# Kernel tuning notes

Hardware: AMD Instinct MI355X
Metric: run time of the kernel (lower is better)

## Reference

```python
import jax, jax.numpy as jnp
import numpy as np

B, U = 64, 512            # batch, max_units
AE = 1024
UE = 256                  # unit_embedding_size
A = 256                   # target_head_attention_size


def setup_inputs() -> dict:
    key = jax.random.key(0)
    ks = jax.random.split(key, 10)
    return {
        "autoregressive_embedding": jax.random.normal(ks[0], (B, U, AE), jnp.float32),
        "own_unit_embeddings": jax.random.normal(ks[1], (B, U, UE), jnp.float32),
        "enemy_unit_embeddings": jax.random.normal(ks[2], (B, U, UE), jnp.float32),
        "nr_own_units": jax.random.randint(ks[3], (B, 1), 0, U).astype(jnp.int64),
        "nr_units_enemy": jax.random.randint(ks[4], (B, 1), 0, U).astype(jnp.int64),
        "nr_own_flags": jax.random.randint(ks[5], (B, 1), 0, 8).astype(jnp.int64),
        "Wq": jax.random.normal(ks[6], (UE + AE, A), jnp.float32) * (1.0 / np.sqrt(UE + AE)),
        "bq": jnp.zeros((A,), jnp.float32),
        "Wk": jax.random.normal(ks[7], (UE, A), jnp.float32) * (1.0 / np.sqrt(UE)),
        "bk": jnp.zeros((A,), jnp.float32),
    }


def reference(autoregressive_embedding, own_unit_embeddings, enemy_unit_embeddings,
              nr_own_units, nr_units_enemy, nr_own_flags, Wq, bq, Wk, bk):
    # combined: [B, U, AE+UE]
    combined = jnp.concatenate([autoregressive_embedding, own_unit_embeddings], axis=2)
    queries = combined @ Wq + bq                       # [B, U, A]
    keys = enemy_unit_embeddings @ Wk + bk             # [B, U, A]
    attention = jnp.einsum("bqd,bkd->bqk", queries, keys) / (A ** 0.5)  # [B, U, U]
    # Vectorized mask: rows in [nr_own_flags, nr_own_units), cols in [0, nr_units_enemy)
    idx = jnp.arange(U)
    row_ok = (idx[None, :] >= nr_own_flags) & (idx[None, :] < nr_own_units)  # [B, U]
    col_ok = idx[None, :] < nr_units_enemy                                   # [B, U]
    mask = jnp.where(row_ok[:, :, None] & col_ok[:, None, :], 1.0, 1e-9)     # [B, U, U]
    return jax.nn.softmax(attention * mask, axis=-1)
```

## Files before the change

### kernel.cpp

```cpp
#include <hip/hip_runtime.h>

constexpr int B  = 64;
constexpr int U  = 512;
constexpr int AE = 1024;
constexpr int UE = 256;
constexpr int A  = 256;
constexpr int KQ = AE + UE;

typedef _Float16 f16x8 __attribute__((ext_vector_type(8)));
typedef float    f32x4 __attribute__((ext_vector_type(4)));

__global__ void prep(const float* __restrict__ Wq, const float* __restrict__ Wk,
                     _Float16* __restrict__ WqT, _Float16* __restrict__ WkT) {
    int idx = blockIdx.x * 256 + threadIdx.x;
    if (idx < KQ * A) {
        int k = idx >> 8, n = idx & 255;
        WqT[(size_t)n * KQ + k] = (_Float16)Wq[idx];
    } else {
        int j = idx - KQ * A;
        if (j < A * A) {
            int k = j >> 8, n = j & 255;
            WkT[(size_t)n * A + k] = (_Float16)Wk[j];
        }
    }
}

__global__ __launch_bounds__(512) void gemm(
    const float* __restrict__ A1, int s1, int split,
    const float* __restrict__ A2, int s2,
    const _Float16* __restrict__ BT,
    const float* __restrict__ bias,
    _Float16* __restrict__ Out,
    int Ktot)
{
    __shared__ __align__(16) _Float16 Al[2][2][64][32];
    __shared__ __align__(16) _Float16 Bl[2][2][256][32];

    const int t    = threadIdx.x;
    const int lane = t & 63;
    const int w    = t >> 6;
    const int mbase = blockIdx.x * 64;

    const int wm = (w & 1) * 32;
    const int wn = (w >> 1) * 64;

    f32x4 acc[2][4] = {};

    const int ar  = t >> 3;
    const int aq  = t & 7;
    const int ap  = aq >> 2;
    const int asw = ((aq & 3) ^ ((ar >> 1) & 3)) * 8;
    const size_t grow = mbase + ar;

    int bp[4], bn[4], bq[4], bsw[4];
    #pragma unroll
    for (int j = 0; j < 4; j++) {
        int s = j * 512 + t;
        bp[j] = s >> 10;
        bn[j] = (s & 1023) >> 2;
        bq[j] = s & 3;
        bsw[j] = ((bq[j] ^ ((bn[j] >> 1) & 3))) * 8;
    }

    float4 areg0, areg1;
    f16x8 breg[4];

    auto loadA = [&](int k0) {
        int kg = k0 + aq * 8;
        const float* src = (kg < split) ? (A1 + grow * (size_t)s1 + kg)
                                        : (A2 + grow * (size_t)s2 + (kg - split));
        areg0 = ((const float4*)src)[0];
        areg1 = ((const float4*)src)[1];
    };
    auto loadB = [&](int k0) {
        #pragma unroll
        for (int j = 0; j < 4; j++)
            breg[j] = *(const f16x8*)(BT + (size_t)bn[j] * Ktot + k0 + bp[j] * 32 + bq[j] * 8);
    };
    auto writeAB = [&](int nb) {
        f16x8 hv;
        hv[0] = (_Float16)areg0.x; hv[1] = (_Float16)areg0.y;
        hv[2] = (_Float16)areg0.z; hv[3] = (_Float16)areg0.w;
        hv[4] = (_Float16)areg1.x; hv[5] = (_Float16)areg1.y;
        hv[6] = (_Float16)areg1.z; hv[7] = (_Float16)areg1.w;
        *(f16x8*)(&Al[nb][ap][ar][asw]) = hv;
        #pragma unroll
        for (int j = 0; j < 4; j++)
            *(f16x8*)(&Bl[nb][bp[j]][bn[j]][bsw[j]]) = breg[j];
    };

    loadA(0);
    loadB(0);
    writeAB(0);
    asm volatile("s_waitcnt lgkmcnt(0)" ::: "memory");
    __builtin_amdgcn_s_barrier();
    __builtin_amdgcn_sched_barrier(0);

    const int rsw = (((lane & 15) >> 1) & 3);
    const int nk = Ktot >> 6;
    int cur = 0;
    for (int kb = 0; kb < nk; kb++) {
        const bool more = (kb + 1 < nk);
        if (more) { loadA(kb * 64 + 64); loadB(kb * 64 + 64); }
        #pragma unroll
        for (int p = 0; p < 2; p++) {
            f16x8 af[2], bf[4];
            #pragma unroll
            for (int mt = 0; mt < 2; mt++)
                af[mt] = *(const f16x8*)(&Al[cur][p][wm + mt * 16 + (lane & 15)][(((lane >> 4) ^ rsw)) * 8]);
            #pragma unroll
            for (int nt = 0; nt < 4; nt++)
                bf[nt] = *(const f16x8*)(&Bl[cur][p][wn + nt * 16 + (lane & 15)][(((lane >> 4) ^ rsw)) * 8]);
            #pragma unroll
            for (int mt = 0; mt < 2; mt++)
                #pragma unroll
                for (int nt = 0; nt < 4; nt++)
                    acc[mt][nt] = __builtin_amdgcn_mfma_f32_16x16x32_f16(
                        af[mt], bf[nt], acc[mt][nt], 0, 0, 0);
        }
        __builtin_amdgcn_sched_barrier(0);
        if (more) writeAB(cur ^ 1);
        asm volatile("s_waitcnt lgkmcnt(0)" ::: "memory");
        __builtin_amdgcn_s_barrier();
        __builtin_amdgcn_sched_barrier(0);
        cur ^= 1;
    }

    const int col0 = wn + (lane & 15);
    const int rsub = (lane >> 4) * 4;
    #pragma unroll
    for (int nt = 0; nt < 4; nt++) {
        const int col = col0 + nt * 16;
        const float bv = bias[col];
        const int c5 = col >> 5, c31 = col & 31;
        #pragma unroll
        for (int mt = 0; mt < 2; mt++)
            #pragma unroll
            for (int r = 0; r < 4; r++) {
                int row = mbase + wm + mt * 16 + rsub + r;
                int bb = row >> 9, u = row & 511;
                Out[(((size_t)bb * 8 + c5) * 512 + u) * 32 + c31] =
                    (_Float16)(acc[mt][nt][r] + bv);
            }
    }
}

__global__ __launch_bounds__(512) void attn(
    const _Float16* __restrict__ Qh, const _Float16* __restrict__ Kh,
    const int* __restrict__ nr_own_units, const int* __restrict__ nr_units_enemy,
    const int* __restrict__ nr_own_flags, float* __restrict__ Out)
{
    __shared__ __align__(16) _Float16 Ql[8][64][32];
    __shared__ __align__(16) _Float16 Kl[512][32];
    __shared__ float red[64][4];

    const int t    = threadIdx.x;
    const int lane = t & 63;
    const int w    = t >> 6;
    const int b    = blockIdx.y;
    const int qbase = blockIdx.x * 64;

    const int nf = nr_own_flags[b];
    const int nu = nr_own_units[b];
    const int ne = nr_units_enemy[b];

    const int wm = (w & 1) * 32;
    const int wn = (w >> 1) * 128;

    f16x8 qreg[4];
    {
        const _Float16* Qb = Qh + ((size_t)b * 8 * 512 + qbase) * 32;
        #pragma unroll
        for (int j = 0; j < 4; j++) {
            int s = j * 512 + t;
            int p = s >> 8, row = (s & 255) >> 2, cq = s & 3;
            qreg[j] = *(const f16x8*)(Qb + ((size_t)p * 512 + row) * 32 + cq * 8);
        }
        #pragma unroll
        for (int j = 0; j < 4; j++) {
            int s = j * 512 + t;
            int p = s >> 8, row = (s & 255) >> 2, cq = s & 3;
            *(f16x8*)(&Ql[p][row][(cq ^ ((row >> 1) & 3)) * 8]) = qreg[j];
        }
    }

    const _Float16* Kb = Kh + (size_t)b * 8 * 512 * 32;
    f16x8 kreg[4];
    const int krow = t >> 2;
    const int kq   = t & 3;
    auto loadK = [&](int c) {
        const _Float16* Kc = Kb + (size_t)c * 512 * 32;
        #pragma unroll
        for (int j = 0; j < 4; j++)
            kreg[j] = *(const f16x8*)(Kc + ((size_t)(j * 128 + krow)) * 32 + kq * 8);
    };
    loadK(0);

    f32x4 acc[2][8] = {};
    const int rsw = (((lane & 15) >> 1) & 3);
    for (int c = 0; c < 8; c++) {
        __syncthreads();
        #pragma unroll
        for (int j = 0; j < 4; j++) {
            int row = j * 128 + krow;
            *(f16x8*)(&Kl[row][(kq ^ ((row >> 1) & 3)) * 8]) = kreg[j];
        }
        __syncthreads();
        if (c < 7) loadK(c + 1);
        f16x8 af[2], bf[8];
        #pragma unroll
        for (int mt = 0; mt < 2; mt++)
            af[mt] = *(const f16x8*)(&Ql[c][wm + mt * 16 + (lane & 15)][((lane >> 4) ^ rsw) * 8]);
        #pragma unroll
        for (int nt = 0; nt < 8; nt++)
            bf[nt] = *(const f16x8*)(&Kl[wn + nt * 16 + (lane & 15)][((lane >> 4) ^ rsw) * 8]);
        #pragma unroll
        for (int mt = 0; mt < 2; mt++)
            #pragma unroll
            for (int nt = 0; nt < 8; nt++)
                acc[mt][nt] = __builtin_amdgcn_mfma_f32_16x16x32_f16(
                    af[mt], bf[nt], acc[mt][nt], 0, 0, 0);
    }

    const int rsub = (lane >> 4) * 4;
    #pragma unroll
    for (int mt = 0; mt < 2; mt++)
        #pragma unroll
        for (int nt = 0; nt < 8; nt++)
            #pragma unroll
            for (int r = 0; r < 4; r++) {
                int rl = wm + mt * 16 + rsub + r;
                int uq = qbase + rl;
                int col = wn + nt * 16 + (lane & 15);
                bool ok = (col < ne) && (uq >= nf) && (uq < nu);
                acc[mt][nt][r] = acc[mt][nt][r] * 0.0625f * (ok ? 1.0f : 1e-9f);
            }

    float mx[2][4];
    #pragma unroll
    for (int mt = 0; mt < 2; mt++)
        #pragma unroll
        for (int r = 0; r < 4; r++) {
            float m = acc[mt][0][r];
            #pragma unroll
            for (int nt = 1; nt < 8; nt++) m = fmaxf(m, acc[mt][nt][r]);
            #pragma unroll
            for (int off = 1; off <= 8; off <<= 1) m = fmaxf(m, __shfl_xor(m, off));
            mx[mt][r] = m;
        }
    if ((lane & 15) == 0) {
        #pragma unroll
        for (int mt = 0; mt < 2; mt++)
            #pragma unroll
            for (int r = 0; r < 4; r++)
                red[wm + mt * 16 + rsub + r][w >> 1] = mx[mt][r];
    }
    __syncthreads();
    #pragma unroll
    for (int mt = 0; mt < 2; mt++)
        #pragma unroll
        for (int r = 0; r < 4; r++) {
            f32x4 v = *(const f32x4*)(&red[wm + mt * 16 + rsub + r][0]);
            mx[mt][r] = fmaxf(fmaxf(v[0], v[1]), fmaxf(v[2], v[3]));
        }
    __syncthreads();

    float sm[2][4];
    #pragma unroll
    for (int mt = 0; mt < 2; mt++)
        #pragma unroll
        for (int r = 0; r < 4; r++) {
            float s = 0.f;
            #pragma unroll
            for (int nt = 0; nt < 8; nt++) {
                float e = __expf(acc[mt][nt][r] - mx[mt][r]);
                acc[mt][nt][r] = e;
                s += e;
            }
            #pragma unroll
            for (int off = 1; off <= 8; off <<= 1) s += __shfl_xor(s, off);
            sm[mt][r] = s;
        }
    if ((lane & 15) == 0) {
        #pragma unroll
        for (int mt = 0; mt < 2; mt++)
            #pragma unroll
            for (int r = 0; r < 4; r++)
                red[wm + mt * 16 + rsub + r][w >> 1] = sm[mt][r];
    }
    __syncthreads();

    #pragma unroll
    for (int mt = 0; mt < 2; mt++)
        #pragma unroll
        for (int r = 0; r < 4; r++) {
            int rl = wm + mt * 16 + rsub + r;
            f32x4 v = *(const f32x4*)(&red[rl][0]);
            float inv = 1.0f / (v[0] + v[1] + v[2] + v[3]);
            float* orow = Out + ((size_t)b * 512 + qbase + rl) * 512 + wn + (lane & 15);
            #pragma unroll
            for (int nt = 0; nt < 8; nt++)
                orow[nt * 16] = acc[mt][nt][r] * inv;
        }
}

extern "C" void kernel_launch(void* const* d_in, const int* in_sizes, int n_in,
                              void* d_out, int out_size, void* d_ws, size_t ws_size,
                              hipStream_t stream) {
    const float* ar    = (const float*)d_in[0];
    const float* own   = (const float*)d_in[1];
    const float* enemy = (const float*)d_in[2];
    const int*   n_own   = (const int*)d_in[3];
    const int*   n_enemy = (const int*)d_in[4];
    const int*   n_flags = (const int*)d_in[5];
    const float* Wq = (const float*)d_in[6];
    const float* bq = (const float*)d_in[7];
    const float* Wk = (const float*)d_in[8];
    const float* bk = (const float*)d_in[9];
    float* out = (float*)d_out;

    char* ws = (char*)d_ws;
    _Float16* WqT = (_Float16*)(ws);
    _Float16* WkT = (_Float16*)(ws + 655360);
    _Float16* Qh  = (_Float16*)(ws + 786432);
    _Float16* Kh  = (_Float16*)(ws + 786432 + 16777216);

    prep<<<dim3((KQ * A + A * A) / 256), dim3(256), 0, stream>>>(Wq, Wk, WqT, WkT);

    gemm<<<dim3(512), dim3(512), 0, stream>>>(ar, AE, AE, own, UE, WqT, bq, Qh, KQ);
    gemm<<<dim3(512), dim3(512), 0, stream>>>(enemy, UE, 0, enemy, UE, WkT, bk, Kh, A);

    attn<<<dim3(8, B), dim3(512), 0, stream>>>(Qh, Kh, n_own, n_enemy, n_flags, out);
}
```

Baseline: 332.3 us.

## Pre-swizzle weight tiles and stage B via direct global-to-LDS loads

The prep kernel now writes the weights in the exact swizzled LDS tile order, so the GEMM can stage B with global_load_lds straight into shared memory and skip the register round trip and per-thread address math. The Q/K outputs are also written pre-swizzled, so the attention kernel copies them into LDS without applying the XOR itself. The cost is a vmcnt(0) wait at each barrier and a tighter coupling of layouts across all three kernels.

```diff
diff --git a/kernel.cpp b/kernel.cpp
--- a/kernel.cpp
+++ b/kernel.cpp
@@ -10,19 +10,22 @@
 typedef _Float16 f16x8 __attribute__((ext_vector_type(8)));
 typedef float    f32x4 __attribute__((ext_vector_type(4)));
 
+
 __global__ void prep(const float* __restrict__ Wq, const float* __restrict__ Wk,
-                     _Float16* __restrict__ WqT, _Float16* __restrict__ WkT) {
+                     _Float16* __restrict__ BTq, _Float16* __restrict__ BTk) {
     int idx = blockIdx.x * 256 + threadIdx.x;
-    if (idx < KQ * A) {
-        int k = idx >> 8, n = idx & 255;
-        WqT[(size_t)n * KQ + k] = (_Float16)Wq[idx];
-    } else {
-        int j = idx - KQ * A;
-        if (j < A * A) {
-            int k = j >> 8, n = j & 255;
-            WkT[(size_t)n * A + k] = (_Float16)Wk[j];
-        }
-    }
+    const float* W;
+    _Float16* Dst;
+    int rem;
+    if (idx < 20 * 2 * 256 * 32) { W = Wq; Dst = BTq; rem = idx; }
+    else                         { W = Wk; Dst = BTk; rem = idx - 20 * 2 * 256 * 32; }
+    int pos = rem & 31;
+    int row = (rem >> 5) & 255;
+    int kp  = rem >> 13;
+    int s = pos >> 3, e = pos & 7;
+    int c = ((s ^ ((row >> 1) & 3)) << 3) | e;
+    int k = kp * 32 + c;
+    Dst[rem] = (_Float16)W[(size_t)k * 256 + row];
 }
 
 __global__ __launch_bounds__(512) void gemm(
@@ -52,18 +55,7 @@
     const int asw = ((aq & 3) ^ ((ar >> 1) & 3)) * 8;
     const size_t grow = mbase + ar;
 
-    int bp[4], bn[4], bq[4], bsw[4];
-    #pragma unroll
-    for (int j = 0; j < 4; j++) {
-        int s = j * 512 + t;
-        bp[j] = s >> 10;
-        bn[j] = (s & 1023) >> 2;
-        bq[j] = s & 3;
-        bsw[j] = ((bq[j] ^ ((bn[j] >> 1) & 3))) * 8;
-    }
-
     float4 areg0, areg1;
-    f16x8 breg[4];
 
     auto loadA = [&](int k0) {
         int kg = k0 + aq * 8;
@@ -72,27 +64,28 @@
         areg0 = ((const float4*)src)[0];
         areg1 = ((const float4*)src)[1];
     };
-    auto loadB = [&](int k0) {
-        #pragma unroll
-        for (int j = 0; j < 4; j++)
-            breg[j] = *(const f16x8*)(BT + (size_t)bn[j] * Ktot + k0 + bp[j] * 32 + bq[j] * 8);
+    auto stageB = [&](int kb, int nb) {
+        const char* g = (const char*)BT + (size_t)kb * 32768 + w * 4096 + (lane << 4);
+        char* l = (char*)(&Bl[nb][0][0][0]) + w * 4096;
+        #pragma unroll
+        for (int i = 0; i < 4; i++)
+            __builtin_amdgcn_global_load_lds(
+                (const __attribute__((address_space(1))) void*)(g + i * 1024),
+                (__attribute__((address_space(3))) void*)(l + i * 1024), 16, 0, 0);
     };
-    auto writeAB = [&](int nb) {
+    auto writeA = [&](int nb) {
         f16x8 hv;
         hv[0] = (_Float16)areg0.x; hv[1] = (_Float16)areg0.y;
         hv[2] = (_Float16)areg0.z; hv[3] = (_Float16)areg0.w;
         hv[4] = (_Float16)areg1.x; hv[5] = (_Float16)areg1.y;
         hv[6] = (_Float16)areg1.z; hv[7] = (_Float16)areg1.w;
         *(f16x8*)(&Al[nb][ap][ar][asw]) = hv;
-        #pragma unroll
-        for (int j = 0; j < 4; j++)
-            *(f16x8*)(&Bl[nb][bp[j]][bn[j]][bsw[j]]) = breg[j];
     };
 
     loadA(0);
-    loadB(0);
-    writeAB(0);
-    asm volatile("s_waitcnt lgkmcnt(0)" ::: "memory");
+    stageB(0, 0);
+    writeA(0);
+    asm volatile("s_waitcnt vmcnt(0) lgkmcnt(0)" ::: "memory");
     __builtin_amdgcn_s_barrier();
     __builtin_amdgcn_sched_barrier(0);
 
@@ -101,7 +94,11 @@
     int cur = 0;
     for (int kb = 0; kb < nk; kb++) {
         const bool more = (kb + 1 < nk);
-        if (more) { loadA(kb * 64 + 64); loadB(kb * 64 + 64); }
+        if (more) {
+            loadA(kb * 64 + 64);
+            stageB(kb + 1, cur ^ 1);
+        }
+        __builtin_amdgcn_sched_barrier(0);
         #pragma unroll
         for (int p = 0; p < 2; p++) {
             f16x8 af[2], bf[4];
@@ -119,8 +116,8 @@
                         af[mt], bf[nt], acc[mt][nt], 0, 0, 0);
         }
         __builtin_amdgcn_sched_barrier(0);
-        if (more) writeAB(cur ^ 1);
-        asm volatile("s_waitcnt lgkmcnt(0)" ::: "memory");
+        if (more) writeA(cur ^ 1);
+        asm volatile("s_waitcnt vmcnt(0) lgkmcnt(0)" ::: "memory");
         __builtin_amdgcn_s_barrier();
         __builtin_amdgcn_sched_barrier(0);
         cur ^= 1;
@@ -133,13 +130,15 @@
         const int col = col0 + nt * 16;
         const float bv = bias[col];
         const int c5 = col >> 5, c31 = col & 31;
+        const int sc = c31 >> 3, ei = c31 & 7;
         #pragma unroll
         for (int mt = 0; mt < 2; mt++)
             #pragma unroll
             for (int r = 0; r < 4; r++) {
                 int row = mbase + wm + mt * 16 + rsub + r;
                 int bb = row >> 9, u = row & 511;
-                Out[(((size_t)bb * 8 + c5) * 512 + u) * 32 + c31] =
+                int posb = ((sc ^ ((u >> 1) & 3)) << 3) | ei;
+                Out[(((size_t)bb * 8 + c5) * 512 + u) * 32 + posb] =
                     (_Float16)(acc[mt][nt][r] + bv);
             }
     }
@@ -180,7 +179,7 @@
         for (int j = 0; j < 4; j++) {
             int s = j * 512 + t;
             int p = s >> 8, row = (s & 255) >> 2, cq = s & 3;
-            *(f16x8*)(&Ql[p][row][(cq ^ ((row >> 1) & 3)) * 8]) = qreg[j];
+            *(f16x8*)(&Ql[p][row][cq * 8]) = qreg[j];
         }
     }
 
@@ -203,7 +202,7 @@
         #pragma unroll
         for (int j = 0; j < 4; j++) {
             int row = j * 128 + krow;
-            *(f16x8*)(&Kl[row][(kq ^ ((row >> 1) & 3)) * 8]) = kreg[j];
+            *(f16x8*)(&Kl[row][kq * 8]) = kreg[j];
         }
         __syncthreads();
         if (c < 7) loadK(c + 1);
@@ -320,15 +319,15 @@
     float* out = (float*)d_out;
 
     char* ws = (char*)d_ws;
-    _Float16* WqT = (_Float16*)(ws);
-    _Float16* WkT = (_Float16*)(ws + 655360);
+    _Float16* BTq = (_Float16*)(ws);
+    _Float16* BTk = (_Float16*)(ws + 655360);
     _Float16* Qh  = (_Float16*)(ws + 786432);
     _Float16* Kh  = (_Float16*)(ws + 786432 + 16777216);
 
-    prep<<<dim3((KQ * A + A * A) / 256), dim3(256), 0, stream>>>(Wq, Wk, WqT, WkT);
-
-    gemm<<<dim3(512), dim3(512), 0, stream>>>(ar, AE, AE, own, UE, WqT, bq, Qh, KQ);
-    gemm<<<dim3(512), dim3(512), 0, stream>>>(enemy, UE, 0, enemy, UE, WkT, bk, Kh, A);
+    prep<<<dim3(1536), dim3(256), 0, stream>>>(Wq, Wk, BTq, BTk);
+
+    gemm<<<dim3(512), dim3(512), 0, stream>>>(ar, AE, AE, own, UE, BTq, bq, Qh, KQ);
+    gemm<<<dim3(512), dim3(512), 0, stream>>>(enemy, UE, 0, enemy, UE, BTk, bk, Kh, A);
 
     attn<<<dim3(8, B), dim3(512), 0, stream>>>(Qh, Kh, n_own, n_enemy, n_flags, out);
 }
```

Measured after the change: 322.6 us. 2.9% less time.
